# Kernel tuning notes

Measured on AMD Instinct MI355X. Metric: run time of the kernel, lower is better.

Reference implementation:

```python
import jax, jax.numpy as jnp
import numpy as np

D = 512; H = 8; HD = D // H; L = 6; QD = 16; MAXLEN = 1000

def _pos_encoding(max_len, d):
    pos = jnp.arange(max_len, dtype=jnp.float32)[:, None]
    div = jnp.exp(jnp.arange(0, d, 2, dtype=jnp.float32) * (-np.log(10000.0) / d))
    pe = jnp.zeros((max_len, d), jnp.float32)
    pe = pe.at[:, 0::2].set(jnp.sin(pos * div))
    pe = pe.at[:, 1::2].set(jnp.cos(pos * div))
    return pe

def _quantum(x, W, b, qwr, qwi, sg, em, mb):
    # QuantumInspiredLayer: classical tanh branch + quantum branch fused by sigmoid gate
    classical = jnp.tanh(x @ W + b)
    qs = x @ sg                          # (B,S,QD) real superposition amplitudes
    ev_r = qs @ qwr                      # complex evolution, real/imag parts kept separate
    ev_i = qs @ qwi
    en_r = ev_r @ em                     # entanglement (real matrix)
    en_i = ev_i @ em
    probs = en_r ** 2 + en_i ** 2        # |entangled|^2, (B,S,QD)
    qout = probs @ mb                    # measurement, (B,S,D)
    fw = jax.nn.sigmoid(jnp.mean(probs, axis=-1, keepdims=True))  # (B,S,1)
    return fw * qout + (1.0 - fw) * classical, probs

def _layer(x, p):
    (Wq, bq, Wk, bk, Wv, bv, Wo, bo,
     qW, qb, qr, qi, qsg, qem, qmb,
     kW, kb, kr, ki, ksg, kem, kmb, g, beta) = p
    B, S, _ = x.shape
    Q = x @ Wq + bq
    K = x @ Wk + bk
    Vv = x @ Wv + bv
    Qq, qp = _quantum(x, qW, qb, qr, qi, qsg, qem, qmb)
    Kq, kp = _quantum(x, kW, kb, kr, ki, ksg, kem, kmb)
    Qf = (0.7 * Q + 0.3 * Qq).reshape(B, S, H, HD).transpose(0, 2, 1, 3)  # (B,H,S,hd)
    Kf = (0.7 * K + 0.3 * Kq).reshape(B, S, H, HD).transpose(0, 2, 1, 3)
    Vh = Vv.reshape(B, S, H, HD).transpose(0, 2, 1, 3)
    scores = jnp.einsum('bhid,bhjd->bhij', Qf, Kf) / np.sqrt(HD).astype(np.float32)
    interf = jnp.einsum('biq,bjq->bij', qp, kp)   # quantum interference term (B,S,S)
    scores = scores + 0.1 * interf[:, None]       # broadcast over heads
    attn = jax.nn.softmax(scores, axis=-1)        # dropout=eval mode (identity)
    ctx = jnp.einsum('bhij,bhjd->bhid', attn, Vh).transpose(0, 2, 1, 3).reshape(B, S, D)
    y = ctx @ Wo + bo + x                         # residual, then LayerNorm
    mu = jnp.mean(y, axis=-1, keepdims=True)
    var = jnp.mean((y - mu) ** 2, axis=-1, keepdims=True)
    y = (y - mu) / jnp.sqrt(var + 1e-5) * g + beta
    return y, attn

def setup_inputs() -> dict:
    key = jax.random.key(0)
    ks = iter(jax.random.split(key, 64))
    def rn(shape, s=0.02):
        return (jax.random.normal(next(ks), shape) * s).astype(jnp.float32)
    B, S, V = 4, 512, 32000
    inp = {
        'text_input': jax.random.randint(next(ks), (B, S), 0, V),
        'visual_input': rn((B, 2048), 1.0),
        'temporal_input': rn((B, 64), 1.0),
        'embed': rn((V, D)),
        'Wvis': rn((2048, D)), 'bvis': jnp.zeros((D,), jnp.float32),
        'Wtemp': rn((64, D)), 'btemp': jnp.zeros((D,), jnp.float32),
        'Wq': rn((L, D, D)), 'bq': jnp.zeros((L, D), jnp.float32),
        'Wk': rn((L, D, D)), 'bk': jnp.zeros((L, D), jnp.float32),
        'Wv': rn((L, D, D)), 'bv': jnp.zeros((L, D), jnp.float32),
        'Wo': rn((L, D, D)), 'bo': jnp.zeros((L, D), jnp.float32),
        'qW': rn((L, D, D)), 'qb': jnp.zeros((L, D), jnp.float32),
        'q_qwr': rn((L, QD, QD), 0.05), 'q_qwi': rn((L, QD, QD), 0.05),
        'q_sg': rn((L, D, QD), 0.05), 'q_em': rn((L, QD, QD), 0.05), 'q_mb': rn((L, QD, D), 0.05),
        'kW': rn((L, D, D)), 'kb': jnp.zeros((L, D), jnp.float32),
        'k_qwr': rn((L, QD, QD), 0.05), 'k_qwi': rn((L, QD, QD), 0.05),
        'k_sg': rn((L, D, QD), 0.05), 'k_em': rn((L, QD, QD), 0.05), 'k_mb': rn((L, QD, D), 0.05),
        'ln_g': jnp.ones((L, D), jnp.float32), 'ln_b': jnp.zeros((L, D), jnp.float32),
        'Ws': rn((D, 64)), 'bs_': jnp.zeros((64,), jnp.float32),
        'Wd': rn((D, 5)), 'bd': jnp.zeros((5,), jnp.float32),
        'We': rn((D, 1)), 'be': jnp.zeros((1,), jnp.float32),
    }
    return inp

def reference(text_input, visual_input, temporal_input, embed, Wvis, bvis, Wtemp, btemp,
              Wq, bq, Wk, bk, Wv, bv, Wo, bo,
              qW, qb, q_qwr, q_qwi, q_sg, q_em, q_mb,
              kW, kb, k_qwr, k_qwi, k_sg, k_em, k_mb,
              ln_g, ln_b, Ws, bs_, Wd, bd, We, be):
    B, S = text_input.shape
    x = (embed[text_input]
         + (visual_input @ Wvis + bvis)[:, None, :]
         + (temporal_input @ Wtemp + btemp)[:, None, :])
    x = x + _pos_encoding(MAXLEN, D)[None, :S, :]
    attns = []
    for l in range(L):
        p = (Wq[l], bq[l], Wk[l], bk[l], Wv[l], bv[l], Wo[l], bo[l],
             qW[l], qb[l], q_qwr[l], q_qwi[l], q_sg[l], q_em[l], q_mb[l],
             kW[l], kb[l], k_qwr[l], k_qwi[l], k_sg[l], k_em[l], k_mb[l],
             ln_g[l], ln_b[l])
        x, a = _layer(x, p)
        attns.append(a)
    pooled = jnp.mean(x, axis=1)  # no attention_mask -> simple mean pool
    skill = jax.nn.sigmoid(pooled @ Ws + bs_)
    diff = jax.nn.softmax(pooled @ Wd + bd, axis=-1)
    eng = jax.nn.sigmoid(pooled @ We + be)
    return skill, diff, eng, x, jnp.stack(attns)
```

## Files before the change

### kernel.cpp

```cpp
#include <hip/hip_runtime.h>
#include <hip/hip_bf16.h>

typedef __attribute__((ext_vector_type(4))) float f32x4;
typedef __attribute__((ext_vector_type(8))) short s16x8;

__device__ __forceinline__ unsigned short f2b(float f) {
  unsigned int u = __float_as_uint(f);
  unsigned int r = (u + 0x7FFFu + ((u >> 16) & 1u)) >> 16;
  return (unsigned short)r;
}
__device__ __forceinline__ float b2f(unsigned short h) {
  return __uint_as_float(((unsigned int)h) << 16);
}
__device__ __forceinline__ void gload16(const void* g, void* l) {
  __builtin_amdgcn_global_load_lds(
      (const __attribute__((address_space(1))) void*)g,
      (__attribute__((address_space(3))) void*)l, 16, 0, 0);
}

enum { MODE_F32 = 0, MODE_VT = 1, MODE_Y = 2 };
struct OutSpec { void* ptr; int mode; };
struct Outs5 { OutSpec o[5]; };
struct Ptr6 { const float* p[6]; };

template<int BM, int BN, int WGM, int WGN>
__global__ __launch_bounds__(256) void gemm_nt(
    const unsigned short* __restrict__ A, int lda, long long strideA,
    const unsigned short* __restrict__ Bm, int ldb, long long strideB,
    const float* __restrict__ biasBase, int biasStride, int perZ,
    Outs5 outs, const float* __restrict__ resid, int K)
{
  constexpr int BK = 32;
  constexpr int WM = BM / WGM, WN = BN / WGN;
  constexpr int WR = WM / 16, WC = WN / 16;
  constexpr int CHA = BM * BK / 8;
  constexpr int CHB = BN * BK / 8;
  __shared__ unsigned short lds_a[2][BM * BK];
  __shared__ unsigned short lds_b[2][BN * BK];
  const int z = blockIdx.z;
  const int tid = threadIdx.x;
  const int wave = tid >> 6, lane = tid & 63;
  const int l16 = lane & 15, lhi = lane >> 4;
  const int wm = (wave / WGN) * WM, wn = (wave % WGN) * WN;
  const int m0 = blockIdx.x * BM, n0 = blockIdx.y * BN;
  const unsigned short* Ap = A + (long long)z * strideA;
  const unsigned short* Bp = Bm + (long long)z * strideB;

  auto stage = [&](int buf, int k0) {
#pragma unroll
    for (int p = 0; p < CHA / 256; ++p) {
      int t = p * 256 + tid;
      gload16(Ap + (long long)(m0 + (t >> 2)) * lda + k0 + (t & 3) * 8, &lds_a[buf][t * 8]);
    }
    if constexpr (CHA % 256) {
      if (tid < CHA % 256) {
        int t = (CHA / 256) * 256 + tid;
        gload16(Ap + (long long)(m0 + (t >> 2)) * lda + k0 + (t & 3) * 8, &lds_a[buf][t * 8]);
      }
    }
#pragma unroll
    for (int p = 0; p < CHB / 256; ++p) {
      int t = p * 256 + tid;
      gload16(Bp + (long long)(n0 + (t >> 2)) * ldb + k0 + (t & 3) * 8, &lds_b[buf][t * 8]);
    }
    if constexpr (CHB % 256) {
      if (tid < CHB % 256) {
        int t = (CHB / 256) * 256 + tid;
        gload16(Bp + (long long)(n0 + (t >> 2)) * ldb + k0 + (t & 3) * 8, &lds_b[buf][t * 8]);
      }
    }
  };

  f32x4 acc[WR][WC];
#pragma unroll
  for (int r = 0; r < WR; ++r)
#pragma unroll
    for (int c = 0; c < WC; ++c) { f32x4 zz = {0.f, 0.f, 0.f, 0.f}; acc[r][c] = zz; }

  stage(0, 0);
  __syncthreads();
  int cur = 0;
  for (int k0 = 0; k0 < K; k0 += BK) {
    if (k0 + BK < K) stage(cur ^ 1, k0 + BK);
    s16x8 af[WR], bfv[WC];
#pragma unroll
    for (int r = 0; r < WR; ++r)
      af[r] = *(const s16x8*)&lds_a[cur][(wm + r * 16 + l16) * BK + lhi * 8];
#pragma unroll
    for (int c = 0; c < WC; ++c)
      bfv[c] = *(const s16x8*)&lds_b[cur][(wn + c * 16 + l16) * BK + lhi * 8];
#pragma unroll
    for (int r = 0; r < WR; ++r)
#pragma unroll
      for (int c = 0; c < WC; ++c)
        acc[r][c] = __builtin_amdgcn_mfma_f32_16x16x32_bf16(af[r], bfv[c], acc[r][c], 0, 0, 0);
    __syncthreads();
    cur ^= 1;
  }

  OutSpec spec = perZ ? outs.o[z] : outs.o[0];
  const float* bias = biasBase ? (biasBase + (long long)z * biasStride) : nullptr;
#pragma unroll
  for (int r = 0; r < WR; ++r) {
#pragma unroll
    for (int c = 0; c < WC; ++c) {
      int n = n0 + wn + c * 16 + l16;
      int rb = m0 + wm + r * 16 + lhi * 4;
      float bv = bias ? bias[n] : 0.f;
      float vv[4];
#pragma unroll
      for (int j = 0; j < 4; ++j) vv[j] = acc[r][c][j] + bv;
      if (spec.mode == MODE_F32) {
#pragma unroll
        for (int j = 0; j < 4; ++j)
          ((float*)spec.ptr)[(long long)(rb + j) * 512 + n] = vv[j];
      } else if (spec.mode == MODE_VT) {
        int b = rb >> 9, s = rb & 511;
        ushort4 pk;
        pk.x = f2b(vv[0]); pk.y = f2b(vv[1]); pk.z = f2b(vv[2]); pk.w = f2b(vv[3]);
        *(ushort4*)&((unsigned short*)spec.ptr)[
            (((long long)(b * 8 + (n >> 6))) * 64 + (n & 63)) * 512 + s] = pk;
      } else {
#pragma unroll
        for (int j = 0; j < 4; ++j)
          ((float*)spec.ptr)[(long long)(rb + j) * 512 + n] =
              vv[j] + resid[(long long)(rb + j) * 512 + n];
      }
    }
  }
}

__global__ __launch_bounds__(256, 1) void fused_attn(
    const unsigned short* __restrict__ Qe, const unsigned short* __restrict__ Ke,
    const unsigned short* __restrict__ Vt, float* __restrict__ attn,
    unsigned short* __restrict__ ctx)
{
  __shared__ unsigned short lds[55296];
  const int z = blockIdx.x, rb = blockIdx.y;
  const int m0 = rb * 64;
  const int b = z >> 3, h = z & 7;
  const int tid = threadIdx.x;
  const int w = tid >> 6, lane = tid & 63;
  const int l16 = lane & 15, lhi = lane >> 4;
  const int rx3 = l16 & 3, rx7 = l16 & 7;

#pragma unroll
  for (int p = 0; p < 3; ++p) {
    int t = p * 256 + tid;
    int row = t / 12, c = t % 12;
    gload16(Qe + ((long long)(z * 512 + m0 + row)) * 96 + (c ^ (row & 3)) * 8, &lds[t * 8]);
  }
#pragma unroll
  for (int p = 0; p < 24; ++p) {
    int t = p * 256 + tid;
    int row = t / 12, c = t % 12;
    gload16(Ke + ((long long)(z * 512 + row)) * 96 + (c ^ (row & 3)) * 8, &lds[6144 + t * 8]);
  }
  __syncthreads();

  const unsigned short* Qs = lds;
  const unsigned short* Ks = lds + 6144;
  s16x8 aq[3];
#pragma unroll
  for (int kk = 0; kk < 3; ++kk)
    aq[kk] = *(const s16x8*)&Qs[(w * 16 + l16) * 96 + (kk * 4 + (lhi ^ rx3)) * 8];
  f32x4 acc[32];
#pragma unroll
  for (int c = 0; c < 32; ++c) { f32x4 zz = {0.f, 0.f, 0.f, 0.f}; acc[c] = zz; }
#pragma unroll
  for (int c = 0; c < 32; ++c) {
#pragma unroll
    for (int kk = 0; kk < 3; ++kk) {
      s16x8 bf = *(const s16x8*)&Ks[(c * 16 + l16) * 96 + (kk * 4 + (lhi ^ rx3)) * 8];
      acc[c] = __builtin_amdgcn_mfma_f32_16x16x32_bf16(aq[kk], bf, acc[c], 0, 0, 0);
    }
  }

  float inv[4];
#pragma unroll
  for (int j = 0; j < 4; ++j) {
    float mx = acc[0][j];
#pragma unroll
    for (int c = 1; c < 32; ++c) mx = fmaxf(mx, acc[c][j]);
    mx = fmaxf(mx, __shfl_xor(mx, 1));
    mx = fmaxf(mx, __shfl_xor(mx, 2));
    mx = fmaxf(mx, __shfl_xor(mx, 4));
    mx = fmaxf(mx, __shfl_xor(mx, 8));
    float sum = 0.f;
#pragma unroll
    for (int c = 0; c < 32; ++c) { float e = __expf(acc[c][j] - mx); acc[c][j] = e; sum += e; }
    sum += __shfl_xor(sum, 1);
    sum += __shfl_xor(sum, 2);
    sum += __shfl_xor(sum, 4);
    sum += __shfl_xor(sum, 8);
    inv[j] = 1.f / sum;
  }
  __syncthreads();

#pragma unroll
  for (int p = 0; p < 8; ++p) {
    int t = p * 256 + tid;
    int row = t >> 5, c = t & 31;
    gload16(Vt + (long long)z * 32768 + row * 512 + (c ^ (row & 7)) * 8, &lds[32768 + t * 8]);
  }
  unsigned short* S = lds;
  {
    float* ap = attn + (long long)z * 262144;
#pragma unroll
    for (int j = 0; j < 4; ++j) {
      int row_l = w * 16 + lhi * 4 + j;
      int rs = row_l & 7;
      float* arow = ap + (long long)(m0 + row_l) * 512;
      unsigned short* srow = S + row_l * 512;
#pragma unroll
      for (int c = 0; c < 32; ++c) {
        float p = acc[c][j] * inv[j];
        int col = c * 16 + l16;
        arow[col] = p;
        srow[((col >> 3) ^ rs) * 8 + (col & 7)] = f2b(p);
      }
    }
  }
  __syncthreads();

  const unsigned short* Vl = lds + 32768;
  f32x4 acc2[4];
#pragma unroll
  for (int c2 = 0; c2 < 4; ++c2) { f32x4 zz = {0.f, 0.f, 0.f, 0.f}; acc2[c2] = zz; }
  const int qrow = w * 16 + l16;
#pragma unroll
  for (int kk = 0; kk < 8; ++kk) {
    s16x8 a = *(const s16x8*)&S[qrow * 512 + ((kk * 4 + lhi) ^ rx7) * 8];
#pragma unroll
    for (int c2 = 0; c2 < 4; ++c2) {
      s16x8 bf = *(const s16x8*)&Vl[(c2 * 16 + l16) * 256 + ((kk * 4 + lhi) ^ rx7) * 8];
      acc2[c2] = __builtin_amdgcn_mfma_f32_16x16x32_bf16(a, bf, acc2[c2], 0, 0, 0);
    }
  }
  __syncthreads();
#pragma unroll
  for (int p = 0; p < 8; ++p) {
    int t = p * 256 + tid;
    int row = t >> 5, c = t & 31;
    gload16(Vt + (long long)z * 32768 + row * 512 + 256 + (c ^ (row & 7)) * 8,
            &lds[32768 + t * 8]);
  }
  __syncthreads();
#pragma unroll
  for (int kk = 8; kk < 16; ++kk) {
    s16x8 a = *(const s16x8*)&S[qrow * 512 + ((kk * 4 + lhi) ^ rx7) * 8];
#pragma unroll
    for (int c2 = 0; c2 < 4; ++c2) {
      s16x8 bf = *(const s16x8*)&Vl[(c2 * 16 + l16) * 256 + (((kk - 8) * 4 + lhi) ^ rx7) * 8];
      acc2[c2] = __builtin_amdgcn_mfma_f32_16x16x32_bf16(a, bf, acc2[c2], 0, 0, 0);
    }
  }
#pragma unroll
  for (int c2 = 0; c2 < 4; ++c2) {
#pragma unroll
    for (int j = 0; j < 4; ++j) {
      int row_g = m0 + w * 16 + lhi * 4 + j;
      ctx[((long long)(b * 512 + row_g)) * 512 + h * 64 + c2 * 16 + l16] = f2b(acc2[c2][j]);
    }
  }
}

__global__ __launch_bounds__(256) void wt_k(Ptr6 srcs, unsigned short* __restrict__ wt) {
  __shared__ float tile[32][33];
  int zz = blockIdx.z;
  int l = zz / 6, mat = zz % 6;
  const float* src = srcs.p[mat] + (long long)l * 262144;
  int tx = threadIdx.x, ty = threadIdx.y;
  int n0 = blockIdx.x * 32, k0 = blockIdx.y * 32;
#pragma unroll
  for (int r = 0; r < 4; ++r)
    tile[ty + r * 8][tx] = src[(long long)(k0 + ty + r * 8) * 512 + n0 + tx];
  __syncthreads();
#pragma unroll
  for (int r = 0; r < 4; ++r)
    wt[(long long)zz * 262144 + (long long)(n0 + ty + r * 8) * 512 + k0 + tx] =
        f2b(tile[tx][ty + r * 8]);
}

__global__ __launch_bounds__(256) void prep_k(Ptr6 biases,
    const float* __restrict__ qwr, const float* __restrict__ qwi, const float* __restrict__ qem,
    const float* __restrict__ kwr, const float* __restrict__ kwi, const float* __restrict__ kem,
    float* __restrict__ biasPacked, float* __restrict__ ArAi) {
  int l = blockIdx.x, t = threadIdx.x;
  for (int m = 0; m < 6; ++m)
    for (int d = t; d < 512; d += 256)
      biasPacked[(l * 6 + m) * 512 + d] = biases.p[m][l * 512 + d];
  int i = t >> 4, j = t & 15;
  const float* em0 = qem + l * 256;
  float ar = 0.f, ai = 0.f;
  for (int tt = 0; tt < 16; ++tt) {
    ar += qwr[l * 256 + i * 16 + tt] * em0[tt * 16 + j];
    ai += qwi[l * 256 + i * 16 + tt] * em0[tt * 16 + j];
  }
  ArAi[(l * 4 + 0) * 256 + t] = ar;
  ArAi[(l * 4 + 1) * 256 + t] = ai;
  const float* em1 = kem + l * 256;
  ar = 0.f; ai = 0.f;
  for (int tt = 0; tt < 16; ++tt) {
    ar += kwr[l * 256 + i * 16 + tt] * em1[tt * 16 + j];
    ai += kwi[l * 256 + i * 16 + tt] * em1[tt * 16 + j];
  }
  ArAi[(l * 4 + 2) * 256 + t] = ar;
  ArAi[(l * 4 + 3) * 256 + t] = ai;
}

__global__ __launch_bounds__(512) void vispart_k(const float* __restrict__ vis,
    const float* __restrict__ Wvis, float* __restrict__ part) {
  int b = blockIdx.x, chunk = blockIdx.y, d = threadIdx.x;
  float acc = 0.f;
  for (int k = chunk * 64; k < chunk * 64 + 64; ++k)
    acc += vis[b * 2048 + k] * Wvis[(long long)k * 512 + d];
  part[(b * 32 + chunk) * 512 + d] = acc;
}
__global__ __launch_bounds__(512) void projsum_k(const float* __restrict__ part,
    const float* __restrict__ bvis, const float* __restrict__ temporal,
    const float* __restrict__ Wtemp, const float* __restrict__ btemp, float* __restrict__ proj) {
  int b = blockIdx.x, d = threadIdx.x;
  float acc = bvis[d] + btemp[d];
  for (int c = 0; c < 32; ++c) acc += part[(b * 32 + c) * 512 + d];
  for (int k = 0; k < 64; ++k) acc += temporal[b * 64 + k] * Wtemp[k * 512 + d];
  proj[b * 512 + d] = acc;
}

__global__ __launch_bounds__(512) void embed_k(const int* __restrict__ text,
    const float* __restrict__ emb, const float* __restrict__ proj,
    float* __restrict__ x, unsigned short* __restrict__ xb) {
  int row = blockIdx.x;
  int b = row >> 9, s = row & 511;
  int d = threadIdx.x;
  int tok = text[row];
  float v = emb[(long long)tok * 512 + d] + proj[b * 512 + d];
  float fr = __expf((float)((d >> 1) << 1) * (-9.2103403719761836f / 512.f));
  float ang = (float)s * fr;
  v += (d & 1) ? cosf(ang) : sinf(ang);
  x[(long long)row * 512 + d] = v;
  xb[(long long)row * 512 + d] = f2b(v);
}

__global__ __launch_bounds__(64) void quantum_k(const float* __restrict__ x,
    const float* __restrict__ sg_q, const float* __restrict__ sg_k,
    const float* __restrict__ ArAiL, float* __restrict__ qp, float* __restrict__ kp,
    float* __restrict__ fwq, float* __restrict__ fwk) {
  int row = blockIdx.x, side = blockIdx.y, lane = threadIdx.x;
  const float* sg = side ? sg_k : sg_q;
  const float* Ar = ArAiL + side * 512;
  const float* Ai = Ar + 256;
  float acc[16];
#pragma unroll
  for (int j = 0; j < 16; ++j) acc[j] = 0.f;
  const float* xr = x + (long long)row * 512;
#pragma unroll
  for (int kk = 0; kk < 8; ++kk) {
    float xv = xr[kk * 64 + lane];
    const float* sgr = sg + (kk * 64 + lane) * 16;
#pragma unroll
    for (int j = 0; j < 16; ++j) acc[j] += xv * sgr[j];
  }
#pragma unroll
  for (int s = 32; s; s >>= 1)
#pragma unroll
    for (int j = 0; j < 16; ++j) acc[j] += __shfl_xor(acc[j], s);
  int j = lane & 15;
  float tr = 0.f, ti = 0.f;
#pragma unroll
  for (int t = 0; t < 16; ++t) {
    tr += acc[t] * Ar[t * 16 + j];
    ti += acc[t] * Ai[t * 16 + j];
  }
  float p = tr * tr + ti * ti;
  float ps = p;
#pragma unroll
  for (int s = 1; s < 16; s <<= 1) ps += __shfl_xor(ps, s);
  if (lane < 16) (side ? kp : qp)[row * 16 + lane] = p;
  if (lane == 0) (side ? fwk : fwq)[row] = 1.f / (1.f + __expf(-ps * (1.f / 16.f)));
}

struct FuseP {
  const float* lin; const float* cl; const float* qp; const float* fw;
  const float* mb; unsigned short* ext; float sA, sB;
};
struct Fuse2 { FuseP s[2]; };
__global__ __launch_bounds__(512) void fuse_k(Fuse2 fp) {
  FuseP P = fp.s[blockIdx.y];
  int row = blockIdx.x;
  int b = row >> 9, i = row & 511;
  int d = threadIdx.x;
  const float* qpr = P.qp + row * 16;
  float fwv = P.fw[row];
  float qout = 0.f;
#pragma unroll
  for (int t = 0; t < 16; ++t) qout += qpr[t] * P.mb[t * 512 + d];
  float qq = fwv * qout + (1.f - fwv) * tanhf(P.cl[(long long)row * 512 + d]);
  float val = (0.7f * P.lin[(long long)row * 512 + d] + 0.3f * qq) * P.sA;
  int h = d >> 6, dd = d & 63;
  P.ext[(((long long)(b * 8 + h)) * 512 + i) * 96 + dd] = f2b(val);
  if (d < 128) {
    int h2 = d >> 4, j = d & 15;
    P.ext[(((long long)(b * 8 + h2)) * 512 + i) * 96 + 64 + j] = f2b(P.sB * qpr[j]);
  } else if (d < 256) {
    int t2 = d - 128;
    int h2 = t2 >> 4, j = t2 & 15;
    P.ext[(((long long)(b * 8 + h2)) * 512 + i) * 96 + 80 + j] = 0;
  }
}

__global__ __launch_bounds__(256) void ln_k(const float* __restrict__ y,
    const float* __restrict__ g, const float* __restrict__ be,
    float* __restrict__ xo, unsigned short* __restrict__ xb, float* __restrict__ xo2) {
  int wv = threadIdx.x >> 6, lane = threadIdx.x & 63;
  long long row = (long long)blockIdx.x * 4 + wv;
  const float* yr = y + row * 512 + lane * 8;
  f32x4 a = *(const f32x4*)yr, b = *(const f32x4*)(yr + 4);
  float s = a[0] + a[1] + a[2] + a[3] + b[0] + b[1] + b[2] + b[3];
#pragma unroll
  for (int m = 32; m; m >>= 1) s += __shfl_xor(s, m);
  float mu = s * (1.f / 512.f);
  float d[8], vs = 0.f;
#pragma unroll
  for (int j = 0; j < 4; ++j) { d[j] = a[j] - mu; vs += d[j] * d[j]; }
#pragma unroll
  for (int j = 0; j < 4; ++j) { d[4 + j] = b[j] - mu; vs += d[4 + j] * d[4 + j]; }
#pragma unroll
  for (int m = 32; m; m >>= 1) vs += __shfl_xor(vs, m);
  float rstd = rsqrtf(vs * (1.f / 512.f) + 1e-5f);
  f32x4 g0 = *(const f32x4*)(g + lane * 8), g1 = *(const f32x4*)(g + lane * 8 + 4);
  f32x4 b0 = *(const f32x4*)(be + lane * 8), b1 = *(const f32x4*)(be + lane * 8 + 4);
  f32x4 o0, o1; s16x8 ob;
#pragma unroll
  for (int j = 0; j < 4; ++j) { o0[j] = d[j] * rstd * g0[j] + b0[j]; ob[j] = (short)f2b(o0[j]); }
#pragma unroll
  for (int j = 0; j < 4; ++j) { o1[j] = d[4 + j] * rstd * g1[j] + b1[j]; ob[4 + j] = (short)f2b(o1[j]); }
  float* xr = xo + row * 512 + lane * 8;
  *(f32x4*)xr = o0; *(f32x4*)(xr + 4) = o1;
  *(s16x8*)(xb + row * 512 + lane * 8) = ob;
  if (xo2) {
    float* x2 = xo2 + row * 512 + lane * 8;
    *(f32x4*)x2 = o0; *(f32x4*)(x2 + 4) = o1;
  }
}

__global__ __launch_bounds__(512) void poolpart_k(const float* __restrict__ x,
                                                   float* __restrict__ part) {
  int b = blockIdx.x, ch = blockIdx.y, d = threadIdx.x;
  float s = 0.f;
  for (int r = 0; r < 64; ++r) s += x[((long long)(b * 512 + ch * 64 + r)) * 512 + d];
  part[(b * 8 + ch) * 512 + d] = s;
}
__global__ __launch_bounds__(512) void head_k(const float* __restrict__ part,
    const float* __restrict__ Ws, const float* __restrict__ bs,
    const float* __restrict__ Wd, const float* __restrict__ bd,
    const float* __restrict__ We, const float* __restrict__ be, float* __restrict__ out) {
  __shared__ float pooled[512];
  __shared__ float dl[5];
  int b = blockIdx.x, d = threadIdx.x;
  float s = 0.f;
  for (int t = 0; t < 8; ++t) s += part[(b * 8 + t) * 512 + d];
  pooled[d] = s * (1.f / 512.f);
  __syncthreads();
  if (d < 64) {
    float a = bs[d];
    for (int t = 0; t < 512; ++t) a += pooled[t] * Ws[t * 64 + d];
    out[b * 64 + d] = 1.f / (1.f + __expf(-a));
  } else if (d < 69) {
    int j = d - 64;
    float a = bd[j];
    for (int t = 0; t < 512; ++t) a += pooled[t] * Wd[t * 5 + j];
    dl[j] = a;
  } else if (d == 69) {
    float a = be[0];
    for (int t = 0; t < 512; ++t) a += pooled[t] * We[t];
    out[276 + b] = 1.f / (1.f + __expf(-a));
  }
  __syncthreads();
  if (d < 5) {
    float mx = dl[0];
    for (int j = 1; j < 5; ++j) mx = fmaxf(mx, dl[j]);
    float sm = 0.f;
    for (int j = 0; j < 5; ++j) sm += __expf(dl[j] - mx);
    out[256 + b * 5 + d] = __expf(dl[d] - mx) / sm;
  }
}

extern "C" void kernel_launch(void* const* d_in, const int* in_sizes, int n_in,
                              void* d_out, int out_size, void* d_ws, size_t ws_size,
                              hipStream_t stream) {
  (void)in_sizes; (void)n_in; (void)out_size; (void)ws_size;
  const int*   text     = (const int*)  d_in[0];
  const float* visual   = (const float*)d_in[1];
  const float* temporal = (const float*)d_in[2];
  const float* embedw   = (const float*)d_in[3];
  const float* Wvis  = (const float*)d_in[4];  const float* bvis  = (const float*)d_in[5];
  const float* Wtemp = (const float*)d_in[6];  const float* btemp = (const float*)d_in[7];
  const float* Wq = (const float*)d_in[8];   const float* bq = (const float*)d_in[9];
  const float* Wk = (const float*)d_in[10];  const float* bk = (const float*)d_in[11];
  const float* Wv = (const float*)d_in[12];  const float* bv = (const float*)d_in[13];
  const float* Wo = (const float*)d_in[14];  const float* bo = (const float*)d_in[15];
  const float* qW = (const float*)d_in[16];  const float* qb = (const float*)d_in[17];
  const float* q_qwr = (const float*)d_in[18]; const float* q_qwi = (const float*)d_in[19];
  const float* q_sg  = (const float*)d_in[20]; const float* q_em  = (const float*)d_in[21];
  const float* q_mb  = (const float*)d_in[22];
  const float* kW = (const float*)d_in[23];  const float* kb = (const float*)d_in[24];
  const float* k_qwr = (const float*)d_in[25]; const float* k_qwi = (const float*)d_in[26];
  const float* k_sg  = (const float*)d_in[27]; const float* k_em  = (const float*)d_in[28];
  const float* k_mb  = (const float*)d_in[29];
  const float* ln_g = (const float*)d_in[30]; const float* ln_b = (const float*)d_in[31];
  const float* Ws = (const float*)d_in[32];  const float* bs_ = (const float*)d_in[33];
  const float* Wd = (const float*)d_in[34];  const float* bd = (const float*)d_in[35];
  const float* We = (const float*)d_in[36];  const float* be = (const float*)d_in[37];
  float* out = (float*)d_out;

  char* w = (char*)d_ws;
  auto alloc = [&](size_t bytes) {
    char* p = w;
    w += (bytes + 255) & ~(size_t)255;
    return p;
  };
  float* ws_x   = (float*)alloc(2048ll * 512 * 4);
  unsigned short* ws_xb = (unsigned short*)alloc(2048ll * 512 * 2);
  unsigned short* ws_Wt = (unsigned short*)alloc(36ll * 262144 * 2);
  float* ws_bias = (float*)alloc(6ll * 6 * 512 * 4);
  float* ws_ArAi = (float*)alloc(6ll * 1024 * 4);
  float* ws_proj = (float*)alloc(4ll * 512 * 4);
  float* ws_vp   = (float*)alloc(4ll * 32 * 512 * 4);
  float* ws_Q    = (float*)alloc(2048ll * 512 * 4);
  float* ws_K    = (float*)alloc(2048ll * 512 * 4);
  float* ws_Cq   = (float*)alloc(2048ll * 512 * 4);
  float* ws_Ck   = (float*)alloc(2048ll * 512 * 4);
  float* ws_qp   = (float*)alloc(2048ll * 16 * 4);
  float* ws_kp   = (float*)alloc(2048ll * 16 * 4);
  float* ws_fwq  = (float*)alloc(2048ll * 4);
  float* ws_fwk  = (float*)alloc(2048ll * 4);
  unsigned short* ws_Vt   = (unsigned short*)alloc(2048ll * 512 * 2);
  unsigned short* ws_Qext = (unsigned short*)alloc(4ll * 8 * 512 * 96 * 2);
  unsigned short* ws_Kext = (unsigned short*)alloc(4ll * 8 * 512 * 96 * 2);
  unsigned short* ws_ctx  = (unsigned short*)alloc(2048ll * 512 * 2);
  float* ws_y    = (float*)alloc(2048ll * 512 * 4);

  Ptr6 wsrc = {{Wq, Wk, Wv, qW, kW, Wo}};
  wt_k<<<dim3(16, 16, 36), dim3(32, 8), 0, stream>>>(wsrc, ws_Wt);
  Ptr6 bsrc = {{bq, bk, bv, qb, kb, bo}};
  prep_k<<<dim3(6), dim3(256), 0, stream>>>(bsrc, q_qwr, q_qwi, q_em, k_qwr, k_qwi, k_em,
                                            ws_bias, ws_ArAi);
  vispart_k<<<dim3(4, 32), dim3(512), 0, stream>>>(visual, Wvis, ws_vp);
  projsum_k<<<dim3(4), dim3(512), 0, stream>>>(ws_vp, bvis, temporal, Wtemp, btemp, ws_proj);
  embed_k<<<dim3(2048), dim3(512), 0, stream>>>(text, embedw, ws_proj, ws_x, ws_xb);

  const long long ATTN_OFF = 280ll + 1048576ll;
  for (int l = 0; l < 6; ++l) {
    const unsigned short* WtL = ws_Wt + (long long)l * 6 * 262144;
    const float* biasL = ws_bias + (long long)l * 6 * 512;

    Outs5 o5{};
    o5.o[0] = { ws_Q, MODE_F32 };  o5.o[1] = { ws_K, MODE_F32 };
    o5.o[2] = { ws_Vt, MODE_VT };  o5.o[3] = { ws_Cq, MODE_F32 };
    o5.o[4] = { ws_Ck, MODE_F32 };
    gemm_nt<128, 128, 2, 2><<<dim3(16, 4, 5), 256, 0, stream>>>(
        ws_xb, 512, 0ll, WtL, 512, 262144ll, biasL, 512, 1, o5, nullptr, 512);

    quantum_k<<<dim3(2048, 2), 64, 0, stream>>>(ws_x, q_sg + l * 8192, k_sg + l * 8192,
        ws_ArAi + l * 1024, ws_qp, ws_kp, ws_fwq, ws_fwk);

    Fuse2 f2{};
    f2.s[0] = { ws_Q, ws_Cq, ws_qp, ws_fwq, q_mb + l * 8192, ws_Qext, 0.125f, 0.1f };
    f2.s[1] = { ws_K, ws_Ck, ws_kp, ws_fwk, k_mb + l * 8192, ws_Kext, 1.0f, 1.0f };
    fuse_k<<<dim3(2048, 2), dim3(512), 0, stream>>>(f2);

    fused_attn<<<dim3(32, 8), 256, 0, stream>>>(
        ws_Qext, ws_Kext, ws_Vt, out + ATTN_OFF + (long long)l * 8388608, ws_ctx);

    Outs5 oy{};
    oy.o[0] = { ws_y, MODE_Y };
    gemm_nt<64, 64, 2, 2><<<dim3(32, 8, 1), 256, 0, stream>>>(
        ws_ctx, 512, 0ll, WtL + 5 * 262144, 512, 0ll, biasL + 5 * 512, 0, 0, oy, ws_x, 512);

    ln_k<<<dim3(512), dim3(256), 0, stream>>>(ws_y, ln_g + l * 512, ln_b + l * 512,
        ws_x, ws_xb, (l == 5) ? (out + 280) : nullptr);
  }

  poolpart_k<<<dim3(4, 8), dim3(512), 0, stream>>>(ws_x, ws_vp);
  head_k<<<dim3(4), dim3(512), 0, stream>>>(ws_vp, Ws, bs_, Wd, bd, We, be, out);
}
```

Before: 507.8 us.

## Store Q/K/classical projections as bf16 and retile the QKV GEMM grid

The fused projection GEMM now writes the Q, K and classical-branch outputs as bf16 instead of fp32, and fuse_k reads them back as bf16. This halves the intermediate traffic. quantum_k now reads the bf16 copy of x with one vectorized 16-byte load per lane instead of fp32 strided loads. The GEMM tile changes from 128x128 to 128x64, doubling the block count to fill more CUs. Rounding the intermediates and x to bf16 adds some precision loss.

```diff
diff --git a/kernel.cpp b/kernel.cpp
--- a/kernel.cpp
+++ b/kernel.cpp
@@ -18,7 +18,7 @@
       (__attribute__((address_space(3))) void*)l, 16, 0, 0);
 }
 
-enum { MODE_F32 = 0, MODE_VT = 1, MODE_Y = 2 };
+enum { MODE_BF16 = 0, MODE_VT = 1, MODE_Y = 2 };
 struct OutSpec { void* ptr; int mode; };
 struct Outs5 { OutSpec o[5]; };
 struct Ptr6 { const float* p[6]; };
@@ -110,10 +110,10 @@
       float vv[4];
 #pragma unroll
       for (int j = 0; j < 4; ++j) vv[j] = acc[r][c][j] + bv;
-      if (spec.mode == MODE_F32) {
+      if (spec.mode == MODE_BF16) {
 #pragma unroll
         for (int j = 0; j < 4; ++j)
-          ((float*)spec.ptr)[(long long)(rb + j) * 512 + n] = vv[j];
+          ((unsigned short*)spec.ptr)[(long long)(rb + j) * 512 + n] = f2b(vv[j]);
       } else if (spec.mode == MODE_VT) {
         int b = rb >> 9, s = rb & 511;
         ushort4 pk;
@@ -342,7 +342,7 @@
   xb[(long long)row * 512 + d] = f2b(v);
 }
 
-__global__ __launch_bounds__(64) void quantum_k(const float* __restrict__ x,
+__global__ __launch_bounds__(64) void quantum_k(const unsigned short* __restrict__ xb,
     const float* __restrict__ sg_q, const float* __restrict__ sg_k,
     const float* __restrict__ ArAiL, float* __restrict__ qp, float* __restrict__ kp,
     float* __restrict__ fwq, float* __restrict__ fwk) {
@@ -353,11 +353,11 @@
   float acc[16];
 #pragma unroll
   for (int j = 0; j < 16; ++j) acc[j] = 0.f;
-  const float* xr = x + (long long)row * 512;
-#pragma unroll
-  for (int kk = 0; kk < 8; ++kk) {
-    float xv = xr[kk * 64 + lane];
-    const float* sgr = sg + (kk * 64 + lane) * 16;
+  s16x8 xv8 = *(const s16x8*)(xb + (long long)row * 512 + lane * 8);
+#pragma unroll
+  for (int e = 0; e < 8; ++e) {
+    float xv = b2f((unsigned short)xv8[e]);
+    const float* sgr = sg + (lane * 8 + e) * 16;
 #pragma unroll
     for (int j = 0; j < 16; ++j) acc[j] += xv * sgr[j];
   }
@@ -381,7 +381,7 @@
 }
 
 struct FuseP {
-  const float* lin; const float* cl; const float* qp; const float* fw;
+  const unsigned short* lin; const unsigned short* cl; const float* qp; const float* fw;
   const float* mb; unsigned short* ext; float sA, sB;
 };
 struct Fuse2 { FuseP s[2]; };
@@ -395,8 +395,8 @@
   float qout = 0.f;
 #pragma unroll
   for (int t = 0; t < 16; ++t) qout += qpr[t] * P.mb[t * 512 + d];
-  float qq = fwv * qout + (1.f - fwv) * tanhf(P.cl[(long long)row * 512 + d]);
-  float val = (0.7f * P.lin[(long long)row * 512 + d] + 0.3f * qq) * P.sA;
+  float qq = fwv * qout + (1.f - fwv) * tanhf(b2f(P.cl[(long long)row * 512 + d]));
+  float val = (0.7f * b2f(P.lin[(long long)row * 512 + d]) + 0.3f * qq) * P.sA;
   int h = d >> 6, dd = d & 63;
   P.ext[(((long long)(b * 8 + h)) * 512 + i) * 96 + dd] = f2b(val);
   if (d < 128) {
@@ -527,10 +527,10 @@
   float* ws_ArAi = (float*)alloc(6ll * 1024 * 4);
   float* ws_proj = (float*)alloc(4ll * 512 * 4);
   float* ws_vp   = (float*)alloc(4ll * 32 * 512 * 4);
-  float* ws_Q    = (float*)alloc(2048ll * 512 * 4);
-  float* ws_K    = (float*)alloc(2048ll * 512 * 4);
-  float* ws_Cq   = (float*)alloc(2048ll * 512 * 4);
-  float* ws_Ck   = (float*)alloc(2048ll * 512 * 4);
+  unsigned short* ws_Q  = (unsigned short*)alloc(2048ll * 512 * 2);
+  unsigned short* ws_K  = (unsigned short*)alloc(2048ll * 512 * 2);
+  unsigned short* ws_Cq = (unsigned short*)alloc(2048ll * 512 * 2);
+  unsigned short* ws_Ck = (unsigned short*)alloc(2048ll * 512 * 2);
   float* ws_qp   = (float*)alloc(2048ll * 16 * 4);
   float* ws_kp   = (float*)alloc(2048ll * 16 * 4);
   float* ws_fwq  = (float*)alloc(2048ll * 4);
@@ -556,13 +556,13 @@
     const float* biasL = ws_bias + (long long)l * 6 * 512;
 
     Outs5 o5{};
-    o5.o[0] = { ws_Q, MODE_F32 };  o5.o[1] = { ws_K, MODE_F32 };
-    o5.o[2] = { ws_Vt, MODE_VT };  o5.o[3] = { ws_Cq, MODE_F32 };
-    o5.o[4] = { ws_Ck, MODE_F32 };
-    gemm_nt<128, 128, 2, 2><<<dim3(16, 4, 5), 256, 0, stream>>>(
+    o5.o[0] = { ws_Q, MODE_BF16 };  o5.o[1] = { ws_K, MODE_BF16 };
+    o5.o[2] = { ws_Vt, MODE_VT };   o5.o[3] = { ws_Cq, MODE_BF16 };
+    o5.o[4] = { ws_Ck, MODE_BF16 };
+    gemm_nt<128, 64, 2, 2><<<dim3(16, 8, 5), 256, 0, stream>>>(
         ws_xb, 512, 0ll, WtL, 512, 262144ll, biasL, 512, 1, o5, nullptr, 512);
 
-    quantum_k<<<dim3(2048, 2), 64, 0, stream>>>(ws_x, q_sg + l * 8192, k_sg + l * 8192,
+    quantum_k<<<dim3(2048, 2), 64, 0, stream>>>(ws_xb, q_sg + l * 8192, k_sg + l * 8192,
         ws_ArAi + l * 1024, ws_qp, ws_kp, ws_fwq, ws_fwk);
 
     Fuse2 f2{};
```

After: 521.9 us. 2.8% more time.

## Split attention key dimension across two wave groups with cross-wave softmax reduction

Applied to the files above, without the earlier changes.

The fused attention kernel now runs 512 threads per block: two groups of four waves each handle half of the 512 keys for the same 64 query rows. Row max and row sum are combined through shared memory, and the partial PV accumulators are reduced through LDS before the bf16 context is written. The full V tile (64x512) now fits in enlarged LDS in one load, which removes the second V reload phase. The goal is more waves per block to hide latency with only 256 blocks, at the cost of extra barriers and LDS traffic.

```diff
diff --git a/kernel.cpp b/kernel.cpp
--- a/kernel.cpp
+++ b/kernel.cpp
@@ -130,12 +130,12 @@
   }
 }
 
-__global__ __launch_bounds__(256, 1) void fused_attn(
+__global__ __launch_bounds__(512, 1) void fused_attn(
     const unsigned short* __restrict__ Qe, const unsigned short* __restrict__ Ke,
     const unsigned short* __restrict__ Vt, float* __restrict__ attn,
     unsigned short* __restrict__ ctx)
 {
-  __shared__ unsigned short lds[55296];
+  __shared__ unsigned short lds[65536];
   const int z = blockIdx.x, rb = blockIdx.y;
   const int m0 = rb * 64;
   const int b = z >> 3, h = z & 7;
@@ -143,16 +143,21 @@
   const int w = tid >> 6, lane = tid & 63;
   const int l16 = lane & 15, lhi = lane >> 4;
   const int rx3 = l16 & 3, rx7 = l16 & 7;
-
-#pragma unroll
-  for (int p = 0; p < 3; ++p) {
-    int t = p * 256 + tid;
+  const int wr = w & 3, kvh = w >> 2;
+
+  {
+    int t = tid;
     int row = t / 12, c = t % 12;
     gload16(Qe + ((long long)(z * 512 + m0 + row)) * 96 + (c ^ (row & 3)) * 8, &lds[t * 8]);
-  }
-#pragma unroll
-  for (int p = 0; p < 24; ++p) {
-    int t = p * 256 + tid;
+    if (tid < 256) {
+      int t2 = 512 + tid;
+      int row2 = t2 / 12, c2 = t2 % 12;
+      gload16(Qe + ((long long)(z * 512 + m0 + row2)) * 96 + (c2 ^ (row2 & 3)) * 8, &lds[t2 * 8]);
+    }
+  }
+#pragma unroll
+  for (int p = 0; p < 12; ++p) {
+    int t = p * 512 + tid;
     int row = t / 12, c = t % 12;
     gload16(Ke + ((long long)(z * 512 + row)) * 96 + (c ^ (row & 3)) * 8, &lds[6144 + t * 8]);
   }
@@ -160,47 +165,64 @@
 
   const unsigned short* Qs = lds;
   const unsigned short* Ks = lds + 6144;
+  float* smax = (float*)&lds[55296];
+  float* ssum = (float*)&lds[55552];
   s16x8 aq[3];
 #pragma unroll
   for (int kk = 0; kk < 3; ++kk)
-    aq[kk] = *(const s16x8*)&Qs[(w * 16 + l16) * 96 + (kk * 4 + (lhi ^ rx3)) * 8];
-  f32x4 acc[32];
-#pragma unroll
-  for (int c = 0; c < 32; ++c) { f32x4 zz = {0.f, 0.f, 0.f, 0.f}; acc[c] = zz; }
-#pragma unroll
-  for (int c = 0; c < 32; ++c) {
+    aq[kk] = *(const s16x8*)&Qs[(wr * 16 + l16) * 96 + (kk * 4 + (lhi ^ rx3)) * 8];
+  f32x4 acc[16];
+#pragma unroll
+  for (int c = 0; c < 16; ++c) { f32x4 zz = {0.f, 0.f, 0.f, 0.f}; acc[c] = zz; }
+#pragma unroll
+  for (int c = 0; c < 16; ++c) {
+    int krow = kvh * 256 + c * 16 + l16;
 #pragma unroll
     for (int kk = 0; kk < 3; ++kk) {
-      s16x8 bf = *(const s16x8*)&Ks[(c * 16 + l16) * 96 + (kk * 4 + (lhi ^ rx3)) * 8];
+      s16x8 bf = *(const s16x8*)&Ks[krow * 96 + (kk * 4 + (lhi ^ rx3)) * 8];
       acc[c] = __builtin_amdgcn_mfma_f32_16x16x32_bf16(aq[kk], bf, acc[c], 0, 0, 0);
     }
   }
 
+#pragma unroll
+  for (int j = 0; j < 4; ++j) {
+    float m = acc[0][j];
+#pragma unroll
+    for (int c = 1; c < 16; ++c) m = fmaxf(m, acc[c][j]);
+    m = fmaxf(m, __shfl_xor(m, 1));
+    m = fmaxf(m, __shfl_xor(m, 2));
+    m = fmaxf(m, __shfl_xor(m, 4));
+    m = fmaxf(m, __shfl_xor(m, 8));
+    if (l16 == 0) smax[kvh * 64 + wr * 16 + lhi * 4 + j] = m;
+  }
+  __syncthreads();
+
+#pragma unroll
+  for (int j = 0; j < 4; ++j) {
+    int r = wr * 16 + lhi * 4 + j;
+    float g = fmaxf(smax[r], smax[64 + r]);
+    float s = 0.f;
+#pragma unroll
+    for (int c = 0; c < 16; ++c) { float e = __expf(acc[c][j] - g); acc[c][j] = e; s += e; }
+    s += __shfl_xor(s, 1);
+    s += __shfl_xor(s, 2);
+    s += __shfl_xor(s, 4);
+    s += __shfl_xor(s, 8);
+    if (l16 == 0) ssum[kvh * 64 + r] = s;
+  }
+  __syncthreads();
   float inv[4];
 #pragma unroll
   for (int j = 0; j < 4; ++j) {
-    float mx = acc[0][j];
-#pragma unroll
-    for (int c = 1; c < 32; ++c) mx = fmaxf(mx, acc[c][j]);
-    mx = fmaxf(mx, __shfl_xor(mx, 1));
-    mx = fmaxf(mx, __shfl_xor(mx, 2));
-    mx = fmaxf(mx, __shfl_xor(mx, 4));
-    mx = fmaxf(mx, __shfl_xor(mx, 8));
-    float sum = 0.f;
-#pragma unroll
-    for (int c = 0; c < 32; ++c) { float e = __expf(acc[c][j] - mx); acc[c][j] = e; sum += e; }
-    sum += __shfl_xor(sum, 1);
-    sum += __shfl_xor(sum, 2);
-    sum += __shfl_xor(sum, 4);
-    sum += __shfl_xor(sum, 8);
-    inv[j] = 1.f / sum;
+    int r = wr * 16 + lhi * 4 + j;
+    inv[j] = 1.f / (ssum[r] + ssum[64 + r]);
   }
   __syncthreads();
 
 #pragma unroll
   for (int p = 0; p < 8; ++p) {
-    int t = p * 256 + tid;
-    int row = t >> 5, c = t & 31;
+    int t = p * 512 + tid;
+    int row = t >> 6, c = t & 63;
     gload16(Vt + (long long)z * 32768 + row * 512 + (c ^ (row & 7)) * 8, &lds[32768 + t * 8]);
   }
   unsigned short* S = lds;
@@ -208,14 +230,14 @@
     float* ap = attn + (long long)z * 262144;
 #pragma unroll
     for (int j = 0; j < 4; ++j) {
-      int row_l = w * 16 + lhi * 4 + j;
+      int row_l = wr * 16 + lhi * 4 + j;
       int rs = row_l & 7;
       float* arow = ap + (long long)(m0 + row_l) * 512;
       unsigned short* srow = S + row_l * 512;
 #pragma unroll
-      for (int c = 0; c < 32; ++c) {
+      for (int c = 0; c < 16; ++c) {
         float p = acc[c][j] * inv[j];
-        int col = c * 16 + l16;
+        int col = kvh * 256 + c * 16 + l16;
         arow[col] = p;
         srow[((col >> 3) ^ rs) * 8 + (col & 7)] = f2b(p);
       }
@@ -227,41 +249,37 @@
   f32x4 acc2[4];
 #pragma unroll
   for (int c2 = 0; c2 < 4; ++c2) { f32x4 zz = {0.f, 0.f, 0.f, 0.f}; acc2[c2] = zz; }
-  const int qrow = w * 16 + l16;
-#pragma unroll
-  for (int kk = 0; kk < 8; ++kk) {
+  const int qrow = wr * 16 + l16;
+#pragma unroll
+  for (int i = 0; i < 8; ++i) {
+    int kk = kvh * 8 + i;
     s16x8 a = *(const s16x8*)&S[qrow * 512 + ((kk * 4 + lhi) ^ rx7) * 8];
 #pragma unroll
     for (int c2 = 0; c2 < 4; ++c2) {
-      s16x8 bf = *(const s16x8*)&Vl[(c2 * 16 + l16) * 256 + ((kk * 4 + lhi) ^ rx7) * 8];
+      s16x8 bf = *(const s16x8*)&Vl[(c2 * 16 + l16) * 512 + ((kk * 4 + lhi) ^ rx7) * 8];
       acc2[c2] = __builtin_amdgcn_mfma_f32_16x16x32_bf16(a, bf, acc2[c2], 0, 0, 0);
     }
   }
   __syncthreads();
-#pragma unroll
-  for (int p = 0; p < 8; ++p) {
-    int t = p * 256 + tid;
-    int row = t >> 5, c = t & 31;
-    gload16(Vt + (long long)z * 32768 + row * 512 + 256 + (c ^ (row & 7)) * 8,
-            &lds[32768 + t * 8]);
-  }
-  __syncthreads();
-#pragma unroll
-  for (int kk = 8; kk < 16; ++kk) {
-    s16x8 a = *(const s16x8*)&S[qrow * 512 + ((kk * 4 + lhi) ^ rx7) * 8];
-#pragma unroll
-    for (int c2 = 0; c2 < 4; ++c2) {
-      s16x8 bf = *(const s16x8*)&Vl[(c2 * 16 + l16) * 256 + (((kk - 8) * 4 + lhi) ^ rx7) * 8];
-      acc2[c2] = __builtin_amdgcn_mfma_f32_16x16x32_bf16(a, bf, acc2[c2], 0, 0, 0);
-    }
-  }
-#pragma unroll
-  for (int c2 = 0; c2 < 4; ++c2) {
-#pragma unroll
-    for (int j = 0; j < 4; ++j) {
-      int row_g = m0 + w * 16 + lhi * 4 + j;
-      ctx[((long long)(b * 512 + row_g)) * 512 + h * 64 + c2 * 16 + l16] = f2b(acc2[c2][j]);
-    }
+
+  float* pb = (float*)lds;
+  if (kvh == 1) {
+#pragma unroll
+    for (int c2 = 0; c2 < 4; ++c2)
+#pragma unroll
+      for (int j = 0; j < 4; ++j)
+        pb[(wr * 16 + lhi * 4 + j) * 64 + c2 * 16 + l16] = acc2[c2][j];
+  }
+  __syncthreads();
+  if (kvh == 0) {
+#pragma unroll
+    for (int c2 = 0; c2 < 4; ++c2)
+#pragma unroll
+      for (int j = 0; j < 4; ++j) {
+        int rl = wr * 16 + lhi * 4 + j;
+        float v = acc2[c2][j] + pb[rl * 64 + c2 * 16 + l16];
+        ctx[((long long)(b * 512 + m0 + rl)) * 512 + h * 64 + c2 * 16 + l16] = f2b(v);
+      }
   }
 }
 
@@ -570,7 +588,7 @@
     f2.s[1] = { ws_K, ws_Ck, ws_kp, ws_fwk, k_mb + l * 8192, ws_Kext, 1.0f, 1.0f };
     fuse_k<<<dim3(2048, 2), dim3(512), 0, stream>>>(f2);
 
-    fused_attn<<<dim3(32, 8), 256, 0, stream>>>(
+    fused_attn<<<dim3(32, 8), 512, 0, stream>>>(
         ws_Qext, ws_Kext, ws_Vt, out + ATTN_OFF + (long long)l * 8388608, ws_ctx);
 
     Outs5 oy{};
```

After: 506.4 us. About the same (-0.3%).
